# Optimization experiments

Hardware: AMD Instinct MI355X
Metric: run time of the kernel (lower is better)

The kernel has to match this reference:

```python
import jax, jax.numpy as jnp
import numpy as np

N_NODES = 100000
K_HOPS = 10
ALPHA = 0.1


def setup_inputs() -> dict:
    key = jax.random.key(0)
    ks = jax.random.split(key, 8)
    x = jax.random.normal(ks[0], (N_NODES, 500), dtype=jnp.float32)
    edge_index = jax.random.randint(ks[1], (2, 1600000), 0, N_NODES, dtype=jnp.int32)
    def glorot(k, shape):
        lim = float(np.sqrt(6.0 / (shape[0] + shape[1])))
        return jax.random.uniform(k, shape, jnp.float32, -lim, lim)
    return {
        "x": x,
        "edge_index": edge_index,
        "W_base": glorot(ks[2], (500, 40)),
        "b_base": jnp.zeros((40,), jnp.float32),
        "W1": glorot(ks[3], (40, 64)),
        "b1": jnp.zeros((64,), jnp.float32),
        "W2": glorot(ks[4], (64, 40)),
        "b2": jnp.zeros((40,), jnp.float32),
    }


def _appnp_propagate(h, edge_index, k, alpha):
    # Symmetrically normalized APPNP: h <- (1-a) * D^-1/2 A D^-1/2 h + a * h0
    src, dst = edge_index[0], edge_index[1]
    E = src.shape[0]
    ones = jnp.ones((E,), h.dtype)
    deg_out = jax.ops.segment_sum(ones, src, num_segments=N_NODES)
    deg_in = jax.ops.segment_sum(ones, dst, num_segments=N_NODES)
    inv_sqrt_out = jnp.where(deg_out > 0, jax.lax.rsqrt(jnp.maximum(deg_out, 1.0)), 0.0)
    inv_sqrt_in = jnp.where(deg_in > 0, jax.lax.rsqrt(jnp.maximum(deg_in, 1.0)), 0.0)
    norm = (inv_sqrt_out[src] * inv_sqrt_in[dst])[:, None]  # [E,1]
    h0 = h

    def body(_, hh):
        msg = hh[src] * norm                 # gather + scale, [E, C]
        agg = jax.ops.segment_sum(msg, dst, num_segments=N_NODES)  # scatter-add
        return (1.0 - alpha) * agg + alpha * h0

    return jax.lax.fori_loop(0, k, body, h0)


def reference(x, edge_index, W_base, b_base, W1, b1, W2, b2):
    # Base model (frozen, no_grad): linear scorer in_channels -> n_classes
    scores = x @ W_base + b_base                     # [N, 40]
    out = jax.nn.softmax(scores, axis=1)
    # ConfGNN MLP: Linear(40->64) + relu, then Linear(64->40)
    h = jax.nn.relu(out @ W1 + b1)
    h = h @ W2 + b2
    adjust_scores = _appnp_propagate(h, edge_index, K_HOPS, ALPHA)
    return adjust_scores, scores
```

## Files before the change

kernel.cpp:

```cpp
#include <hip/hip_runtime.h>

#define N_NODES 100000
#define N_EDGES 1600000
#define QNODES 25000
#define NPASS 4
#define CAP_Q 24
#define NB1 391

typedef __attribute__((ext_vector_type(8))) short short8;
typedef __attribute__((ext_vector_type(4))) float floatx4;

__device__ inline short bf16_rne(float f) {
    union { float f; unsigned u; } v; v.f = f;
    unsigned r = v.u + 0x7FFF + ((v.u >> 16) & 1);
    return (short)(r >> 16);
}

__global__ __launch_bounds__(256) void wt_kernel(
    const float* __restrict__ Wb, const float* __restrict__ W1,
    const float* __restrict__ W2,
    short* __restrict__ WT, short* __restrict__ W1T, short* __restrict__ W2T)
{
    int i = blockIdx.x * 256 + threadIdx.x;
    if (i < 48 * 512) {
        int m = i >> 9, k = i & 511;
        WT[i] = bf16_rne((m < 40 && k < 500) ? Wb[k * 40 + m] : 0.f);
    }
    if (i < 64 * 64) {
        int m = i >> 6, k = i & 63;
        W1T[i] = bf16_rne((k < 40) ? W1[k * 64 + m] : 0.f);
    }
    if (i < 48 * 64) {
        int m = i >> 6, k = i & 63;
        W2T[i] = bf16_rne((m < 40) ? W2[k * 40 + m] : 0.f);
    }
}

__global__ __launch_bounds__(256) void scores_kernel(
    const float* __restrict__ x, const short8* __restrict__ WT8,
    const float* __restrict__ bb, float* __restrict__ scores)
{
    int wave = threadIdx.x >> 6;
    int lane = threadIdx.x & 63;
    int n0 = (blockIdx.x * 4 + wave) * 16;
    if (n0 >= N_NODES) return;
    int n = n0 + (lane & 15);
    int quad = lane >> 4;
    int m = lane & 15;
    const float* xrow = x + (size_t)n * 500 + quad * 8;

    floatx4 acc0 = {0,0,0,0}, acc1 = {0,0,0,0}, acc2 = {0,0,0,0};

    #pragma unroll 5
    for (int ks = 0; ks < 15; ++ks) {
        int k0 = ks * 32;
        float4 xa = *(const float4*)(xrow + k0);
        float4 xb = *(const float4*)(xrow + k0 + 4);
        short8 bf;
        bf[0] = bf16_rne(xa.x); bf[1] = bf16_rne(xa.y);
        bf[2] = bf16_rne(xa.z); bf[3] = bf16_rne(xa.w);
        bf[4] = bf16_rne(xb.x); bf[5] = bf16_rne(xb.y);
        bf[6] = bf16_rne(xb.z); bf[7] = bf16_rne(xb.w);
        int widx = (k0 >> 3) + quad;
        short8 a0 = WT8[(size_t)(0  + m) * 64 + widx];
        short8 a1 = WT8[(size_t)(16 + m) * 64 + widx];
        short8 a2 = WT8[(size_t)(32 + m) * 64 + widx];
        acc0 = __builtin_amdgcn_mfma_f32_16x16x32_bf16(a0, bf, acc0, 0, 0, 0);
        acc1 = __builtin_amdgcn_mfma_f32_16x16x32_bf16(a1, bf, acc1, 0, 0, 0);
        acc2 = __builtin_amdgcn_mfma_f32_16x16x32_bf16(a2, bf, acc2, 0, 0, 0);
    }
    {
        int kbase = 480 + quad * 8;
        float4 xa = {0,0,0,0}, xb = {0,0,0,0};
        if (kbase + 8 <= 500) { xa = *(const float4*)(xrow + 480); xb = *(const float4*)(xrow + 484); }
        else if (kbase < 500) { xa = *(const float4*)(xrow + 480); }
        short8 bf;
        bf[0] = bf16_rne(xa.x); bf[1] = bf16_rne(xa.y);
        bf[2] = bf16_rne(xa.z); bf[3] = bf16_rne(xa.w);
        bf[4] = bf16_rne(xb.x); bf[5] = bf16_rne(xb.y);
        bf[6] = bf16_rne(xb.z); bf[7] = bf16_rne(xb.w);
        int widx = 60 + quad;
        short8 a0 = WT8[(size_t)(0  + m) * 64 + widx];
        short8 a1 = WT8[(size_t)(16 + m) * 64 + widx];
        short8 a2 = WT8[(size_t)(32 + m) * 64 + widx];
        acc0 = __builtin_amdgcn_mfma_f32_16x16x32_bf16(a0, bf, acc0, 0, 0, 0);
        acc1 = __builtin_amdgcn_mfma_f32_16x16x32_bf16(a1, bf, acc1, 0, 0, 0);
        acc2 = __builtin_amdgcn_mfma_f32_16x16x32_bf16(a2, bf, acc2, 0, 0, 0);
    }

    float* srow = scores + (size_t)n * 40;
    int mb = quad * 4;
    float4 b4 = *(const float4*)(bb + mb);
    *(float4*)(srow + mb) = make_float4(acc0[0] + b4.x, acc0[1] + b4.y,
                                        acc0[2] + b4.z, acc0[3] + b4.w);
    mb = 16 + quad * 4;
    b4 = *(const float4*)(bb + mb);
    *(float4*)(srow + mb) = make_float4(acc1[0] + b4.x, acc1[1] + b4.y,
                                        acc1[2] + b4.z, acc1[3] + b4.w);
    mb = 32 + quad * 4;
    if (mb < 40) {
        b4 = *(const float4*)(bb + mb);
        *(float4*)(srow + mb) = make_float4(acc2[0] + b4.x, acc2[1] + b4.y,
                                            acc2[2] + b4.z, acc2[3] + b4.w);
    }
}

__global__ __launch_bounds__(320) void mlp_kernel(
    const float* __restrict__ scores,
    const short8* __restrict__ W1T8, const float* __restrict__ b1,
    const short8* __restrict__ W2T8, const float* __restrict__ b2,
    float* __restrict__ h0, float* __restrict__ u0,
    const float* __restrict__ inv_out)
{
    __shared__ short hs[5][16 * 72];
    int wave = threadIdx.x >> 6;
    int lane = threadIdx.x & 63;
    int q = lane >> 4;
    int n16 = lane & 15;
    int node = (blockIdx.x * 5 + wave) * 16 + n16;
    float iv = inv_out[node];

    const float* srow = scores + (size_t)node * 40;
    float4 xa = *(const float4*)(srow + q * 8);
    float4 xb = *(const float4*)(srow + q * 8 + 4);
    float4 xc = {0,0,0,0}, xd = {0,0,0,0};
    if (q == 0) { xc = *(const float4*)(srow + 32); xd = *(const float4*)(srow + 36); }

    float m = fmaxf(fmaxf(fmaxf(xa.x, xa.y), fmaxf(xa.z, xa.w)),
                    fmaxf(fmaxf(xb.x, xb.y), fmaxf(xb.z, xb.w)));
    if (q == 0)
        m = fmaxf(m, fmaxf(fmaxf(fmaxf(xc.x, xc.y), fmaxf(xc.z, xc.w)),
                           fmaxf(fmaxf(xd.x, xd.y), fmaxf(xd.z, xd.w))));
    m = fmaxf(m, __shfl_xor(m, 16));
    m = fmaxf(m, __shfl_xor(m, 32));

    float e0 = __expf(xa.x - m), e1 = __expf(xa.y - m), e2 = __expf(xa.z - m), e3 = __expf(xa.w - m);
    float e4 = __expf(xb.x - m), e5 = __expf(xb.y - m), e6 = __expf(xb.z - m), e7 = __expf(xb.w - m);
    float f0 = 0, f1 = 0, f2 = 0, f3 = 0, f4 = 0, f5 = 0, f6 = 0, f7 = 0;
    if (q == 0) {
        f0 = __expf(xc.x - m); f1 = __expf(xc.y - m); f2 = __expf(xc.z - m); f3 = __expf(xc.w - m);
        f4 = __expf(xd.x - m); f5 = __expf(xd.y - m); f6 = __expf(xd.z - m); f7 = __expf(xd.w - m);
    }
    float sum = e0 + e1 + e2 + e3 + e4 + e5 + e6 + e7 + f0 + f1 + f2 + f3 + f4 + f5 + f6 + f7;
    sum += __shfl_xor(sum, 16);
    sum += __shfl_xor(sum, 32);
    float inv = 1.f / sum;

    short8 bf_a, bf_b;
    bf_a[0] = bf16_rne(e0 * inv); bf_a[1] = bf16_rne(e1 * inv);
    bf_a[2] = bf16_rne(e2 * inv); bf_a[3] = bf16_rne(e3 * inv);
    bf_a[4] = bf16_rne(e4 * inv); bf_a[5] = bf16_rne(e5 * inv);
    bf_a[6] = bf16_rne(e6 * inv); bf_a[7] = bf16_rne(e7 * inv);
    bf_b[0] = bf16_rne(f0 * inv); bf_b[1] = bf16_rne(f1 * inv);
    bf_b[2] = bf16_rne(f2 * inv); bf_b[3] = bf16_rne(f3 * inv);
    bf_b[4] = bf16_rne(f4 * inv); bf_b[5] = bf16_rne(f5 * inv);
    bf_b[6] = bf16_rne(f6 * inv); bf_b[7] = bf16_rne(f7 * inv);

    short* hw = &hs[wave][0];
    #pragma unroll
    for (int t = 0; t < 4; ++t) {
        floatx4 acc = {0, 0, 0, 0};
        short8 A0 = W1T8[(t * 16 + n16) * 8 + q];
        short8 A1 = W1T8[(t * 16 + n16) * 8 + 4 + q];
        acc = __builtin_amdgcn_mfma_f32_16x16x32_bf16(A0, bf_a, acc, 0, 0, 0);
        acc = __builtin_amdgcn_mfma_f32_16x16x32_bf16(A1, bf_b, acc, 0, 0, 0);
        float4 bv = *(const float4*)(b1 + t * 16 + q * 4);
        short4 pk;
        pk.x = bf16_rne(fmaxf(acc[0] + bv.x, 0.f));
        pk.y = bf16_rne(fmaxf(acc[1] + bv.y, 0.f));
        pk.z = bf16_rne(fmaxf(acc[2] + bv.z, 0.f));
        pk.w = bf16_rne(fmaxf(acc[3] + bv.w, 0.f));
        *(short4*)(hw + n16 * 72 + t * 16 + q * 4) = pk;
    }
    __syncthreads();

    short8 h1a = *(const short8*)(hw + n16 * 72 + q * 8);
    short8 h1b = *(const short8*)(hw + n16 * 72 + 32 + q * 8);

    #pragma unroll
    for (int t = 0; t < 3; ++t) {
        floatx4 acc = {0, 0, 0, 0};
        short8 A0 = W2T8[(t * 16 + n16) * 8 + q];
        short8 A1 = W2T8[(t * 16 + n16) * 8 + 4 + q];
        acc = __builtin_amdgcn_mfma_f32_16x16x32_bf16(A0, h1a, acc, 0, 0, 0);
        acc = __builtin_amdgcn_mfma_f32_16x16x32_bf16(A1, h1b, acc, 0, 0, 0);
        int mc = t * 16 + q * 4;
        if (mc < 40) {
            float4 bv = *(const float4*)(b2 + mc);
            float rx = acc[0] + bv.x, ry = acc[1] + bv.y;
            float rz = acc[2] + bv.z, rw = acc[3] + bv.w;
            size_t idx = (size_t)node * 10 + t * 4 + q;
            ((float4*)h0)[idx] = make_float4(0.1f * rx, 0.1f * ry, 0.1f * rz, 0.1f * rw);
            ((float4*)u0)[idx] = make_float4(iv * rx, iv * ry, iv * rz, iv * rw);
        }
    }
}

__global__ __launch_bounds__(256) void build_kernel(
    const int* __restrict__ src, const int* __restrict__ dst,
    int* __restrict__ deg_out, int* __restrict__ cnt, int* __restrict__ csr2)
{
    int e = blockIdx.x * 256 + threadIdx.x;
    if (e < N_EDGES) {
        int s = src[e], d = dst[e];
        atomicAdd(&deg_out[s], 1);
        int qt = s / QNODES;
        int off = atomicAdd(&cnt[qt * N_NODES + d], 1);
        if (off < CAP_Q) csr2[(size_t)(qt * CAP_Q + off) * N_NODES + d] = s * 10;
    }
}

__global__ __launch_bounds__(256) void inv_kernel(
    const int* __restrict__ deg_out, const int* __restrict__ cnt,
    float* __restrict__ inv_out, float* __restrict__ inv_in)
{
    int i = blockIdx.x * 256 + threadIdx.x;
    if (i < N_NODES) {
        int a = deg_out[i];
        int b = cnt[i] + cnt[N_NODES + i] + cnt[2 * N_NODES + i] + cnt[3 * N_NODES + i];
        inv_out[i] = (a > 0) ? rsqrtf((float)a) : 0.f;
        inv_in[i]  = (b > 0) ? rsqrtf((float)b) : 0.f;
    }
}

__global__ __launch_bounds__(256) void hop_kernel(
    const float4* __restrict__ ucur, const float4* __restrict__ h0,
    const int* __restrict__ cnt, const int* __restrict__ csr2,
    const float* __restrict__ inv_in, const float* __restrict__ inv_out,
    float4* __restrict__ unew, int last)
{
    int gid = blockIdx.x * 256 + threadIdx.x;
    if (gid >= 10 * N_NODES) return;
    int d = gid / 10;
    int q = gid - d * 10;

    float4 acc = make_float4(0.f, 0.f, 0.f, 0.f);

    #pragma unroll
    for (int p = 0; p < NPASS; ++p) {
        const int* col = csr2 + (size_t)p * CAP_Q * N_NODES + d;
        int len = cnt[p * N_NODES + d];
        if (len > CAP_Q) len = CAP_Q;
        int j = 0;
        for (; j + 4 <= len; j += 4) {
            int s0 = col[(size_t)(j + 0) * N_NODES];
            int s1 = col[(size_t)(j + 1) * N_NODES];
            int s2 = col[(size_t)(j + 2) * N_NODES];
            int s3 = col[(size_t)(j + 3) * N_NODES];
            float4 v0 = ucur[s0 + q];
            float4 v1 = ucur[s1 + q];
            float4 v2 = ucur[s2 + q];
            float4 v3 = ucur[s3 + q];
            acc.x += (v0.x + v1.x) + (v2.x + v3.x);
            acc.y += (v0.y + v1.y) + (v2.y + v3.y);
            acc.z += (v0.z + v1.z) + (v2.z + v3.z);
            acc.w += (v0.w + v1.w) + (v2.w + v3.w);
        }
        for (; j < len; ++j) {
            int s = col[(size_t)j * N_NODES];
            float4 v = ucur[s + q];
            acc.x += v.x; acc.y += v.y; acc.z += v.z; acc.w += v.w;
        }
    }

    float4 h0v = h0[gid];
    float wi = 0.9f * inv_in[d];
    float4 res = make_float4(h0v.x + wi * acc.x, h0v.y + wi * acc.y,
                             h0v.z + wi * acc.z, h0v.w + wi * acc.w);
    if (!last) {
        float io = inv_out[d];
        res = make_float4(io * res.x, io * res.y, io * res.z, io * res.w);
    }
    unew[gid] = res;
}

extern "C" void kernel_launch(void* const* d_in, const int* in_sizes, int n_in,
                              void* d_out, int out_size, void* d_ws, size_t ws_size,
                              hipStream_t stream) {
    const float* x  = (const float*)d_in[0];
    const int*   ei = (const int*)d_in[1];
    const int*   src = ei;
    const int*   dst = ei + N_EDGES;
    const float* Wb = (const float*)d_in[2];
    const float* bb = (const float*)d_in[3];
    const float* W1 = (const float*)d_in[4];
    const float* b1 = (const float*)d_in[5];
    const float* W2 = (const float*)d_in[6];
    const float* b2 = (const float*)d_in[7];

    float* out_adj    = (float*)d_out;
    float* out_scores = (float*)d_out + 4000000;

    float* h0      = (float*)d_ws;
    float* uA      = h0 + 4000000;
    int* deg_out   = (int*)(uA + 4000000);
    int* cnt       = deg_out + N_NODES;
    float* inv_o   = (float*)(cnt + 4 * N_NODES);
    float* inv_i   = inv_o + N_NODES;
    int* csr2      = (int*)(inv_i + N_NODES);
    short* WT      = (short*)(csr2 + (size_t)NPASS * CAP_Q * N_NODES);
    short* W1T     = WT + 48 * 512;
    short* W2T     = W1T + 64 * 64;

    hipMemsetAsync(deg_out, 0, 5 * N_NODES * sizeof(int), stream);

    build_kernel<<<N_EDGES / 256, 256, 0, stream>>>(src, dst, deg_out, cnt, csr2);
    inv_kernel<<<NB1, 256, 0, stream>>>(deg_out, cnt, inv_o, inv_i);

    wt_kernel<<<96, 256, 0, stream>>>(Wb, W1, W2, WT, W1T, W2T);
    scores_kernel<<<1563, 256, 0, stream>>>(
        x, (const short8*)WT, bb, out_scores);
    mlp_kernel<<<1250, 320, 0, stream>>>(
        out_scores, (const short8*)W1T, b1, (const short8*)W2T, b2,
        h0, out_adj, inv_o);

    int nblk = (10 * N_NODES + 255) / 256;
    for (int k = 0; k < 10; ++k) {
        const float* cur = (k & 1) ? uA : out_adj;
        float* nxt       = (k & 1) ? out_adj : uA;
        int last = (k == 9);
        hop_kernel<<<nblk, 256, 0, stream>>>(
            (const float4*)cur, (const float4*)h0, cnt, csr2,
            inv_i, inv_o, (float4*)nxt, last);
    }
}
```

Before: 932.6 us.

## Store propagated features in bf16 and fuse graph build with scores GEMM

```diff
diff --git a/kernel.cpp b/kernel.cpp
--- a/kernel.cpp
+++ b/kernel.cpp
@@ -6,6 +6,8 @@
 #define NPASS 4
 #define CAP_Q 24
 #define NB1 391
+#define SCORES_BLKS 1563
+#define BUILD_BLKS 6250
 
 typedef __attribute__((ext_vector_type(8))) short short8;
 typedef __attribute__((ext_vector_type(4))) float floatx4;
@@ -15,6 +17,10 @@
     unsigned r = v.u + 0x7FFF + ((v.u >> 16) & 1);
     return (short)(r >> 16);
 }
+__device__ inline float bf2f(unsigned short h) {
+    union { unsigned u; float f; } v; v.u = (unsigned)h << 16;
+    return v.f;
+}
 
 __global__ __launch_bounds__(256) void wt_kernel(
     const float* __restrict__ Wb, const float* __restrict__ W1,
@@ -36,10 +42,24 @@
     }
 }
 
-__global__ __launch_bounds__(256) void scores_kernel(
+__global__ __launch_bounds__(256) void mega_kernel(
     const float* __restrict__ x, const short8* __restrict__ WT8,
-    const float* __restrict__ bb, float* __restrict__ scores)
-{
+    const float* __restrict__ bb, float* __restrict__ scores,
+    const int* __restrict__ src, const int* __restrict__ dst,
+    int* __restrict__ deg_out, int* __restrict__ cnt, int* __restrict__ csr2)
+{
+    if (blockIdx.x >= SCORES_BLKS) {
+        int e = (blockIdx.x - SCORES_BLKS) * 256 + threadIdx.x;
+        if (e < N_EDGES) {
+            int s = src[e], d = dst[e];
+            atomicAdd(&deg_out[s], 1);
+            int qt = s / QNODES;
+            int off = atomicAdd(&cnt[qt * N_NODES + d], 1);
+            if (off < CAP_Q) csr2[(size_t)(qt * CAP_Q + off) * N_NODES + d] = s * 10;
+        }
+        return;
+    }
+
     int wave = threadIdx.x >> 6;
     int lane = threadIdx.x & 63;
     int n0 = (blockIdx.x * 4 + wave) * 16;
@@ -105,11 +125,24 @@
     }
 }
 
+__global__ __launch_bounds__(256) void inv_kernel(
+    const int* __restrict__ deg_out, const int* __restrict__ cnt,
+    float* __restrict__ inv_out, float* __restrict__ inv_in)
+{
+    int i = blockIdx.x * 256 + threadIdx.x;
+    if (i < N_NODES) {
+        int a = deg_out[i];
+        int b = cnt[i] + cnt[N_NODES + i] + cnt[2 * N_NODES + i] + cnt[3 * N_NODES + i];
+        inv_out[i] = (a > 0) ? rsqrtf((float)a) : 0.f;
+        inv_in[i]  = (b > 0) ? rsqrtf((float)b) : 0.f;
+    }
+}
+
 __global__ __launch_bounds__(320) void mlp_kernel(
     const float* __restrict__ scores,
     const short8* __restrict__ W1T8, const float* __restrict__ b1,
     const short8* __restrict__ W2T8, const float* __restrict__ b2,
-    float* __restrict__ h0, float* __restrict__ u0,
+    float* __restrict__ h0, ushort4* __restrict__ u0,
     const float* __restrict__ inv_out)
 {
     __shared__ short hs[5][16 * 72];
@@ -191,43 +224,21 @@
             float rz = acc[2] + bv.z, rw = acc[3] + bv.w;
             size_t idx = (size_t)node * 10 + t * 4 + q;
             ((float4*)h0)[idx] = make_float4(0.1f * rx, 0.1f * ry, 0.1f * rz, 0.1f * rw);
-            ((float4*)u0)[idx] = make_float4(iv * rx, iv * ry, iv * rz, iv * rw);
+            ushort4 pk;
+            pk.x = (unsigned short)bf16_rne(iv * rx);
+            pk.y = (unsigned short)bf16_rne(iv * ry);
+            pk.z = (unsigned short)bf16_rne(iv * rz);
+            pk.w = (unsigned short)bf16_rne(iv * rw);
+            u0[idx] = pk;
         }
     }
 }
 
-__global__ __launch_bounds__(256) void build_kernel(
-    const int* __restrict__ src, const int* __restrict__ dst,
-    int* __restrict__ deg_out, int* __restrict__ cnt, int* __restrict__ csr2)
-{
-    int e = blockIdx.x * 256 + threadIdx.x;
-    if (e < N_EDGES) {
-        int s = src[e], d = dst[e];
-        atomicAdd(&deg_out[s], 1);
-        int qt = s / QNODES;
-        int off = atomicAdd(&cnt[qt * N_NODES + d], 1);
-        if (off < CAP_Q) csr2[(size_t)(qt * CAP_Q + off) * N_NODES + d] = s * 10;
-    }
-}
-
-__global__ __launch_bounds__(256) void inv_kernel(
-    const int* __restrict__ deg_out, const int* __restrict__ cnt,
-    float* __restrict__ inv_out, float* __restrict__ inv_in)
-{
-    int i = blockIdx.x * 256 + threadIdx.x;
-    if (i < N_NODES) {
-        int a = deg_out[i];
-        int b = cnt[i] + cnt[N_NODES + i] + cnt[2 * N_NODES + i] + cnt[3 * N_NODES + i];
-        inv_out[i] = (a > 0) ? rsqrtf((float)a) : 0.f;
-        inv_in[i]  = (b > 0) ? rsqrtf((float)b) : 0.f;
-    }
-}
-
 __global__ __launch_bounds__(256) void hop_kernel(
-    const float4* __restrict__ ucur, const float4* __restrict__ h0,
+    const ushort4* __restrict__ ucur, const float4* __restrict__ h0,
     const int* __restrict__ cnt, const int* __restrict__ csr2,
     const float* __restrict__ inv_in, const float* __restrict__ inv_out,
-    float4* __restrict__ unew, int last)
+    ushort4* __restrict__ unew, float4* __restrict__ outf, int last)
 {
     int gid = blockIdx.x * 256 + threadIdx.x;
     if (gid >= 10 * N_NODES) return;
@@ -247,19 +258,20 @@
             int s1 = col[(size_t)(j + 1) * N_NODES];
             int s2 = col[(size_t)(j + 2) * N_NODES];
             int s3 = col[(size_t)(j + 3) * N_NODES];
-            float4 v0 = ucur[s0 + q];
-            float4 v1 = ucur[s1 + q];
-            float4 v2 = ucur[s2 + q];
-            float4 v3 = ucur[s3 + q];
-            acc.x += (v0.x + v1.x) + (v2.x + v3.x);
-            acc.y += (v0.y + v1.y) + (v2.y + v3.y);
-            acc.z += (v0.z + v1.z) + (v2.z + v3.z);
-            acc.w += (v0.w + v1.w) + (v2.w + v3.w);
+            ushort4 v0 = ucur[s0 + q];
+            ushort4 v1 = ucur[s1 + q];
+            ushort4 v2 = ucur[s2 + q];
+            ushort4 v3 = ucur[s3 + q];
+            acc.x += (bf2f(v0.x) + bf2f(v1.x)) + (bf2f(v2.x) + bf2f(v3.x));
+            acc.y += (bf2f(v0.y) + bf2f(v1.y)) + (bf2f(v2.y) + bf2f(v3.y));
+            acc.z += (bf2f(v0.z) + bf2f(v1.z)) + (bf2f(v2.z) + bf2f(v3.z));
+            acc.w += (bf2f(v0.w) + bf2f(v1.w)) + (bf2f(v2.w) + bf2f(v3.w));
         }
         for (; j < len; ++j) {
             int s = col[(size_t)j * N_NODES];
-            float4 v = ucur[s + q];
-            acc.x += v.x; acc.y += v.y; acc.z += v.z; acc.w += v.w;
+            ushort4 v = ucur[s + q];
+            acc.x += bf2f(v.x); acc.y += bf2f(v.y);
+            acc.z += bf2f(v.z); acc.w += bf2f(v.w);
         }
     }
 
@@ -267,11 +279,17 @@
     float wi = 0.9f * inv_in[d];
     float4 res = make_float4(h0v.x + wi * acc.x, h0v.y + wi * acc.y,
                              h0v.z + wi * acc.z, h0v.w + wi * acc.w);
-    if (!last) {
+    if (last) {
+        outf[gid] = res;
+    } else {
         float io = inv_out[d];
-        res = make_float4(io * res.x, io * res.y, io * res.z, io * res.w);
-    }
-    unew[gid] = res;
+        ushort4 pk;
+        pk.x = (unsigned short)bf16_rne(io * res.x);
+        pk.y = (unsigned short)bf16_rne(io * res.y);
+        pk.z = (unsigned short)bf16_rne(io * res.z);
+        pk.w = (unsigned short)bf16_rne(io * res.w);
+        unew[gid] = pk;
+    }
 }
 
 extern "C" void kernel_launch(void* const* d_in, const int* in_sizes, int n_in,
@@ -292,8 +310,9 @@
     float* out_scores = (float*)d_out + 4000000;
 
     float* h0      = (float*)d_ws;
-    float* uA      = h0 + 4000000;
-    int* deg_out   = (int*)(uA + 4000000);
+    ushort* ubfA   = (ushort*)(h0 + 4000000);
+    ushort* ubfB   = ubfA + 4000000;
+    int* deg_out   = (int*)(ubfB + 4000000);
     int* cnt       = deg_out + N_NODES;
     float* inv_o   = (float*)(cnt + 4 * N_NODES);
     float* inv_i   = inv_o + N_NODES;
@@ -304,23 +323,23 @@
 
     hipMemsetAsync(deg_out, 0, 5 * N_NODES * sizeof(int), stream);
 
-    build_kernel<<<N_EDGES / 256, 256, 0, stream>>>(src, dst, deg_out, cnt, csr2);
+    wt_kernel<<<96, 256, 0, stream>>>(Wb, W1, W2, WT, W1T, W2T);
+    mega_kernel<<<SCORES_BLKS + BUILD_BLKS, 256, 0, stream>>>(
+        x, (const short8*)WT, bb, out_scores,
+        src, dst, deg_out, cnt, csr2);
     inv_kernel<<<NB1, 256, 0, stream>>>(deg_out, cnt, inv_o, inv_i);
 
-    wt_kernel<<<96, 256, 0, stream>>>(Wb, W1, W2, WT, W1T, W2T);
-    scores_kernel<<<1563, 256, 0, stream>>>(
-        x, (const short8*)WT, bb, out_scores);
     mlp_kernel<<<1250, 320, 0, stream>>>(
         out_scores, (const short8*)W1T, b1, (const short8*)W2T, b2,
-        h0, out_adj, inv_o);
+        h0, (ushort4*)ubfA, inv_o);
 
     int nblk = (10 * N_NODES + 255) / 256;
     for (int k = 0; k < 10; ++k) {
-        const float* cur = (k & 1) ? uA : out_adj;
-        float* nxt       = (k & 1) ? out_adj : uA;
+        const ushort4* cur = (const ushort4*)((k & 1) ? ubfB : ubfA);
+        ushort4* nxt       = (ushort4*)((k & 1) ? ubfA : ubfB);
         int last = (k == 9);
         hop_kernel<<<nblk, 256, 0, stream>>>(
-            (const float4*)cur, (const float4*)h0, cnt, csr2,
-            inv_i, inv_o, (float4*)nxt, last);
-    }
-}
+            cur, (const float4*)h0, cnt, csr2,
+            inv_i, inv_o, nxt, (float4*)out_adj, last);
+    }
+}
```

Measured after the change: 830.2 us. 11.0% less time.
